# Kernel optimization log

Hardware: AMD Instinct MI355X
Metric: run time of the kernel (lower is better)

Reference implementation:

```python
import jax, jax.numpy as jnp
from jax import lax
import numpy as np

C_IN, D_INNER, D_STATE, OUT_CH = 20, 32, 8, 20
DT_RANK = max(1, D_INNER // 8)
B, H, W = 4, 384, 384
EPS = 1e-5


def layernorm(x, g, b):
    m = jnp.mean(x, axis=-1, keepdims=True)
    v = jnp.mean((x - m) ** 2, axis=-1, keepdims=True)
    return (x - m) * lax.rsqrt(v + EPS) * g + b


def ss1d(x, xw, dw, db, A_log, Dp):
    # x: (Bb, L, Dd). Mamba selective scan: h_t = exp(dt*A)*h_{t-1} + dt*B_t*u_t; y_t = C_t.h_t + D*u_t
    Bb, L, Dd = x.shape
    N = A_log.shape[1]
    xdbl = x @ xw.T                                   # (Bb, L, dtr+2N)
    dt_lo, Bm, Cm = jnp.split(xdbl, [DT_RANK, DT_RANK + N], axis=-1)
    dt = jax.nn.softplus(dt_lo @ dw.T + db)           # (Bb, L, Dd)
    A = -jnp.exp(A_log)                               # (Dd, N)

    def step(h, inp):
        dt_t, B_t, C_t, u_t = inp                     # (Bb,Dd),(Bb,N),(Bb,N),(Bb,Dd)
        dA = jnp.exp(dt_t[:, :, None] * A)            # (Bb, Dd, N)
        h = dA * h + (dt_t * u_t)[:, :, None] * B_t[:, None, :]
        y = jnp.einsum('bdn,bn->bd', h, C_t)
        return h, y

    xs = (jnp.moveaxis(dt, 1, 0), jnp.moveaxis(Bm, 1, 0),
          jnp.moveaxis(Cm, 1, 0), jnp.moveaxis(x, 1, 0))
    h0 = jnp.zeros((Bb, Dd, N), dtype=x.dtype)
    _, ys = lax.scan(step, h0, xs)
    return jnp.moveaxis(ys, 0, 1) + x * Dp


def setup_inputs() -> dict:
    key = jax.random.key(0)
    ks = jax.random.split(key, 16)
    s = lambda k, shp, sc=0.05: jax.random.normal(k, shp, dtype=jnp.float32) * sc
    A_log1 = jnp.log(jnp.broadcast_to(jnp.arange(1, D_STATE + 1, dtype=jnp.float32), (D_INNER, D_STATE)))
    return {
        'x': jax.random.normal(ks[0], (B, C_IN, H, W), dtype=jnp.float32),
        'norm_g': jnp.ones((C_IN,), jnp.float32),
        'norm_b': jnp.zeros((C_IN,), jnp.float32),
        'inproj_w': s(ks[1], (D_INNER, C_IN), 0.15),
        'dw_w': s(ks[2], (3, 3, 1, D_INNER), 0.2),
        'dw_b': jnp.zeros((D_INNER,), jnp.float32),
        'ssm_xw': s(ks[3], (4, DT_RANK + 2 * D_STATE, D_INNER), 0.1),
        'ssm_dw': s(ks[4], (4, D_INNER, DT_RANK), 0.5),
        'ssm_db': s(ks[5], (4, D_INNER), 0.5) - 3.0,
        'ssm_Alog': jnp.broadcast_to(A_log1, (4, D_INNER, D_STATE)).copy(),
        'ssm_D': jnp.ones((4, D_INNER), jnp.float32),
        'merge_g': jnp.ones((4 * D_INNER,), jnp.float32),
        'merge_b': jnp.zeros((4 * D_INNER,), jnp.float32),
        'merge_w': s(ks[6], (D_INNER, 4 * D_INNER), 0.1),
        'out_w': s(ks[7], (OUT_CH, D_INNER), 0.15),
        'out_b': jnp.zeros((OUT_CH,), jnp.float32),
    }


def reference(x, norm_g, norm_b, inproj_w, dw_w, dw_b, ssm_xw, ssm_dw, ssm_db,
              ssm_Alog, ssm_D, merge_g, merge_b, merge_w, out_w, out_b):
    Bx, C, Hx, Wx = x.shape
    h = jnp.transpose(x, (0, 2, 3, 1))                      # (B,H,W,C)
    h = layernorm(h, norm_g, norm_b)
    h = jax.nn.silu(h @ inproj_w.T)                          # (B,H,W,Dd)
    h = lax.conv_general_dilated(h, dw_w, (1, 1), 'SAME',
                                 dimension_numbers=('NHWC', 'HWIO', 'NHWC'),
                                 feature_group_count=D_INNER) + dw_b
    h = jax.nn.silu(h)                                       # (B,H,W,Dd)

    p = lambda i: (ssm_xw[i], ssm_dw[i], ssm_db[i], ssm_Alog[i], ssm_D[i])

    x_h = h.reshape(Bx * Hx, Wx, D_INNER)
    y_h_fwd = ss1d(x_h, *p(0)).reshape(Bx, Hx, Wx, D_INNER)
    y_h_bwd = ss1d(x_h[:, ::-1], *p(1))[:, ::-1].reshape(Bx, Hx, Wx, D_INNER)

    x_v = jnp.transpose(h, (0, 2, 1, 3)).reshape(Bx * Wx, Hx, D_INNER)
    y_v_fwd = jnp.transpose(ss1d(x_v, *p(2)).reshape(Bx, Wx, Hx, D_INNER), (0, 2, 1, 3))
    y_v_bwd = jnp.transpose(ss1d(x_v[:, ::-1], *p(3))[:, ::-1].reshape(Bx, Wx, Hx, D_INNER), (0, 2, 1, 3))

    y = jnp.concatenate([y_h_fwd, y_h_bwd, y_v_fwd, y_v_bwd], axis=-1)  # (B,H,W,4*Dd)
    y = layernorm(y, merge_g, merge_b)
    y = y @ merge_w.T                                        # (B,H,W,Dd)
    y = y @ out_w.T + out_b                                  # (B,H,W,out_ch)
    return jnp.transpose(y, (0, 3, 1, 2))                    # (B,out_ch,H,W)
```

## Files before the change

### kernel.cpp

```cpp
#include <hip/hip_runtime.h>

typedef unsigned short u16;
typedef unsigned int   u32;
typedef unsigned long long u64;
typedef float f2 __attribute__((ext_vector_type(2)));

#define CIN  20
#define DIN  32
#define BB   4
#define HH   384
#define WW   384
#define HW   147456
#define BHW  589824
#define EPSF 1e-5f
#define GUARD 65536

__device__ __forceinline__ float bflo(u32 u) {
    union { u32 v; float f; } x; x.v = u << 16; return x.f;
}
__device__ __forceinline__ float bfhi(u32 u) {
    union { u32 v; float f; } x; x.v = u & 0xffff0000u; return x.f;
}
__device__ __forceinline__ float bf2f(u16 h) {
    union { u32 v; float f; } x; x.v = ((u32)h) << 16; return x.f;
}
__device__ __forceinline__ u16 f2bf(float f) {
    union { float f; u32 u; } v; v.f = f;
    u32 u = v.u;
    return (u16)((u + 0x7FFFu + ((u >> 16) & 1u)) >> 16);
}
__device__ __forceinline__ float silu_f(float a) {
    return a / (1.f + __expf(-a));
}
__device__ __forceinline__ float softplus_f(float z) {
    return (z > 15.f) ? z : __logf(1.f + __expf(z));
}

__global__ void k_prep(const float* __restrict__ ow, const float* __restrict__ mw,
                       const float* __restrict__ mg, const float* __restrict__ mb,
                       const float* __restrict__ ob,
                       float* __restrict__ Wt, float* __restrict__ rsum,
                       float* __restrict__ c0)
{
    __shared__ float mdot[DIN];
    int t = threadIdx.x;
    if (t < DIN) {
        float s = 0.f;
        for (int k = 0; k < 128; ++k) s += mw[t*128 + k] * mb[k];
        mdot[t] = s;
    }
    {
        int k = t;
        for (int o = 0; o < CIN; ++o) {
            float s = 0.f;
            for (int d = 0; d < DIN; ++d) s += ow[o*DIN + d] * mw[d*128 + k];
            Wt[k*CIN + o] = s * mg[k];
        }
    }
    __syncthreads();
    if (t < CIN) {
        float rs = 0.f;
        for (int k = 0; k < 128; ++k) rs += Wt[k*CIN + t];
        rsum[t] = rs;
        float c = ob[t];
        for (int d = 0; d < DIN; ++d) c += ow[t*DIN + d] * mdot[d];
        c0[t] = c;
    }
}

__global__ __launch_bounds__(256) void k_lnproj(
    const float* __restrict__ x, const float* __restrict__ ng,
    const float* __restrict__ nb, const float* __restrict__ ipw,
    u16* __restrict__ h1)
{
    __shared__ float w_s[DIN*CIN];
    __shared__ float g_s[CIN], b_s[CIN];
    for (int i = threadIdx.x; i < DIN*CIN; i += 256) w_s[i] = ipw[i];
    if (threadIdx.x < CIN) { g_s[threadIdx.x] = ng[threadIdx.x]; b_s[threadIdx.x] = nb[threadIdx.x]; }
    __syncthreads();

    int p = blockIdx.x*256 + threadIdx.x;
    int b = p / HW, rem = p % HW;
    float v[CIN];
    float m = 0.f;
    #pragma unroll
    for (int c = 0; c < CIN; ++c) { v[c] = x[(b*CIN + c)*HW + rem]; m += v[c]; }
    m *= (1.f/CIN);
    float var = 0.f;
    #pragma unroll
    for (int c = 0; c < CIN; ++c) { float d = v[c]-m; var += d*d; }
    var *= (1.f/CIN);
    float rstd = rsqrtf(var + EPSF);
    #pragma unroll
    for (int c = 0; c < CIN; ++c) v[c] = (v[c]-m)*rstd*g_s[c] + b_s[c];

    float o[DIN];
    #pragma unroll
    for (int j = 0; j < DIN; ++j) {
        float acc = 0.f;
        #pragma unroll
        for (int c = 0; c < CIN; ++c) acc += w_s[j*CIN + c]*v[c];
        o[j] = silu_f(acc);
    }
    u32 pk[16];
    #pragma unroll
    for (int j2 = 0; j2 < 16; ++j2)
        pk[j2] = (u32)f2bf(o[2*j2]) | ((u32)f2bf(o[2*j2+1]) << 16);
    uint4* dst = (uint4*)(h1 + (size_t)p*DIN);
    dst[0] = make_uint4(pk[0],pk[1],pk[2],pk[3]);
    dst[1] = make_uint4(pk[4],pk[5],pk[6],pk[7]);
    dst[2] = make_uint4(pk[8],pk[9],pk[10],pk[11]);
    dst[3] = make_uint4(pk[12],pk[13],pk[14],pk[15]);
}

__global__ __launch_bounds__(256) void k_conv(
    const u16* __restrict__ h1, const float* __restrict__ cw,
    const float* __restrict__ cb, u16* __restrict__ h2)
{
    __shared__ float w_s[9*DIN];
    __shared__ float b_s[DIN];
    for (int i = threadIdx.x; i < 9*DIN; i += 256) w_s[i] = cw[i];
    if (threadIdx.x < DIN) b_s[threadIdx.x] = cb[threadIdx.x];
    __syncthreads();

    int tid = blockIdx.x*256 + threadIdx.x;
    int p = tid >> 2, g = tid & 3;
    int b = p / HW, rem = p % HW;
    int yy0 = rem / WW, xx0 = rem % WW;

    float acc[8];
    #pragma unroll
    for (int i = 0; i < 8; ++i) acc[i] = b_s[g*8 + i];

    #pragma unroll
    for (int dy = -1; dy <= 1; ++dy) {
        int yy = yy0 + dy;
        #pragma unroll
        for (int dx = -1; dx <= 1; ++dx) {
            int xc = xx0 + dx;
            if (yy >= 0 && yy < HH && xc >= 0 && xc < WW) {
                uint4 q = *(const uint4*)(h1 + ((size_t)(b*HW + yy*WW + xc)*DIN + g*8));
                int k = (dy+1)*3 + (dx+1);
                const float* wp = &w_s[k*DIN + g*8];
                acc[0] += wp[0]*bflo(q.x);  acc[1] += wp[1]*bfhi(q.x);
                acc[2] += wp[2]*bflo(q.y);  acc[3] += wp[3]*bfhi(q.y);
                acc[4] += wp[4]*bflo(q.z);  acc[5] += wp[5]*bfhi(q.z);
                acc[6] += wp[6]*bflo(q.w);  acc[7] += wp[7]*bfhi(q.w);
            }
        }
    }
    u32 pk[4];
    #pragma unroll
    for (int i2 = 0; i2 < 4; ++i2) {
        float a = silu_f(acc[2*i2]);
        float c = silu_f(acc[2*i2+1]);
        pk[i2] = (u32)f2bf(a) | ((u32)f2bf(c) << 16);
    }
    *(uint4*)(h2 + ((size_t)p*DIN + g*8)) = make_uint4(pk[0],pk[1],pk[2],pk[3]);
}

__global__ __launch_bounds__(256) void k_proj(
    const u16* __restrict__ h2, const float* __restrict__ xw,
    u16* __restrict__ dlA, u16* __restrict__ bcA)
{
    __shared__ float xw_s[4*CIN*DIN];
    for (int i = threadIdx.x; i < 4*CIN*DIN; i += 256) xw_s[i] = xw[i];
    __syncthreads();

    int p = blockIdx.x*256 + threadIdx.x;
    float u[DIN];
    const uint4* src = (const uint4*)(h2 + (size_t)p*DIN);
    #pragma unroll
    for (int q4 = 0; q4 < 4; ++q4) {
        uint4 v = src[q4];
        u[q4*8+0]=bflo(v.x); u[q4*8+1]=bfhi(v.x);
        u[q4*8+2]=bflo(v.y); u[q4*8+3]=bfhi(v.y);
        u[q4*8+4]=bflo(v.z); u[q4*8+5]=bfhi(v.z);
        u[q4*8+6]=bflo(v.w); u[q4*8+7]=bfhi(v.w);
    }
    #pragma unroll 1
    for (int dir = 0; dir < 4; ++dir) {
        float xd[CIN];
        #pragma unroll
        for (int j = 0; j < CIN; ++j) xd[j] = 0.f;
        #pragma unroll
        for (int d4 = 0; d4 < 8; ++d4) {
            float u0 = u[d4*4], u1 = u[d4*4+1], u2 = u[d4*4+2], u3 = u[d4*4+3];
            #pragma unroll
            for (int j = 0; j < CIN; ++j) {
                float4 w4 = *(const float4*)&xw_s[(dir*CIN + j)*DIN + d4*4];
                xd[j] += w4.x*u0 + w4.y*u1 + w4.z*u2 + w4.w*u3;
            }
        }
        u32 pk[10];
        #pragma unroll
        for (int i = 0; i < 10; ++i)
            pk[i] = (u32)f2bf(xd[2*i]) | ((u32)f2bf(xd[2*i+1]) << 16);
        *(uint2*)(dlA + (size_t)(dir*BHW + p)*4) = make_uint2(pk[0], pk[1]);
        uint4* bcd = (uint4*)(bcA + (size_t)(dir*BHW + p)*16);
        bcd[0] = make_uint4(pk[2], pk[3], pk[4], pk[5]);
        bcd[1] = make_uint4(pk[6], pk[7], pk[8], pk[9]);
    }
}

__global__ __launch_bounds__(256) void k_scan(
    const char* __restrict__ h2b,
    const char* __restrict__ dlb_,
    const char* __restrict__ bcb_,
    const float* __restrict__ Alog, const float* __restrict__ Dp,
    const float* __restrict__ dwm,  const float* __restrict__ dbv,
    char* __restrict__ y4b)
{
    int tid  = blockIdx.x*256 + threadIdx.x;
    int wv   = tid >> 6, lane = tid & 63;
    int half = lane >> 5, d = lane & 31;
    int dir  = wv / 768;
    int s    = (wv % 768)*2 + half;
    int b    = s / 384, r = s % 384;

    int p0, stp;
    if (dir == 0)      { p0 = b*HW + r*WW;           stp = 1;  }
    else if (dir == 1) { p0 = b*HW + r*WW + (WW-1);  stp = -1; }
    else if (dir == 2) { p0 = b*HW + r;              stp = WW; }
    else               { p0 = b*HW + (HH-1)*WW + r;  stp = -WW;}

    float Av[8];
    bool okl = true;
    #pragma unroll
    for (int j = 0; j < 8; ++j) {
        float e = __expf(Alog[(dir*DIN + d)*8 + j]);
        Av[j] = -e;
        okl = okl && (__builtin_fabsf(e - (float)(j+1)) < 2e-3f);
    }
    bool fast = (__ballot(okl) == ~0ull);

    float Dd  = Dp[dir*DIN + d];
    float dw0 = dwm[(dir*DIN + d)*4 + 0], dw1 = dwm[(dir*DIN + d)*4 + 1];
    float dw2 = dwm[(dir*DIN + d)*4 + 2], dw3 = dwm[(dir*DIN + d)*4 + 3];
    float dbc = dbv[dir*DIN + d];

    u32 uo = GUARD + (u32)((p0*DIN + d)*2);            int su = stp*DIN*2;
    u32 yo = (u32)((dir*BHW + p0)*64 + d*2);           int sy = stp*64;
    u32 c1 = GUARD + (u32)((dir*BHW + p0)*8);          int s1 = stp*8;
    u32 c2 = GUARD + (u32)((dir*BHW + p0)*32);         int s2 = stp*32;

    u16 ub[2]; uint2 dlr[2]; uint4 B4[2], C4[2];
    u32 fu = uo, f1 = c1, f2o = c2;

    auto fetch = [&](int sl) {
        ub[sl]  = *(const u16*)(h2b + fu);
        dlr[sl] = *(const uint2*)(dlb_ + f1);
        B4[sl]  = *(const uint4*)(bcb_ + f2o);
        C4[sl]  = *(const uint4*)(bcb_ + f2o + 16);
        fu += (u32)su; f1 += (u32)s1; f2o += (u32)s2;
    };

    fetch(0); fetch(1);

    f2 h0 = {0.f,0.f}, h1 = {0.f,0.f}, h2v = {0.f,0.f}, h3 = {0.f,0.f};

    if (fast) {
        #pragma unroll 2
        for (int t = 0; t < 384; ++t) {
            int sl = t & 1;
            float uu = bf2f(ub[sl]);
            uint2 dl = dlr[sl];
            uint4 Bv = B4[sl], Cv = C4[sl];
            fetch(sl);

            float z = dbc + dw0*bflo(dl.x) + dw1*bfhi(dl.x)
                          + dw2*bflo(dl.y) + dw3*bfhi(dl.y);
            z = fminf(z, 80.f);
            float rr = __builtin_amdgcn_rcpf(1.f + __expf(z));
            float dt = -__logf(rr);
            float r2 = rr*rr;
            f2 rr2 = {r2, r2};
            f2 a01 = {rr, r2};
            f2 a23 = a01*rr2;
            f2 a45 = a23*rr2;
            f2 a67 = a45*rr2;

            float dtu = dt*uu;
            f2 du2 = {dtu, dtu};
            f2 Bp0 = { bflo(Bv.x), bfhi(Bv.x) }, Bp1 = { bflo(Bv.y), bfhi(Bv.y) };
            f2 Bp2 = { bflo(Bv.z), bfhi(Bv.z) }, Bp3 = { bflo(Bv.w), bfhi(Bv.w) };
            f2 Cp0 = { bflo(Cv.x), bfhi(Cv.x) }, Cp1 = { bflo(Cv.y), bfhi(Cv.y) };
            f2 Cp2 = { bflo(Cv.z), bfhi(Cv.z) }, Cp3 = { bflo(Cv.w), bfhi(Cv.w) };

            h0  = __builtin_elementwise_fma(a01, h0,  du2*Bp0);
            h1  = __builtin_elementwise_fma(a23, h1,  du2*Bp1);
            h2v = __builtin_elementwise_fma(a45, h2v, du2*Bp2);
            h3  = __builtin_elementwise_fma(a67, h3,  du2*Bp3);

            f2 yv = Cp0*h0;
            yv = __builtin_elementwise_fma(Cp1, h1,  yv);
            yv = __builtin_elementwise_fma(Cp2, h2v, yv);
            yv = __builtin_elementwise_fma(Cp3, h3,  yv);

            float y = yv.x + yv.y + Dd*uu;
            *(u16*)(y4b + yo) = f2bf(y);
            yo += (u32)sy;
        }
    } else {
        f2 A2[4];
        #pragma unroll
        for (int j = 0; j < 4; ++j) { A2[j].x = Av[2*j]; A2[j].y = Av[2*j+1]; }
        #pragma unroll 2
        for (int t = 0; t < 384; ++t) {
            int sl = t & 1;
            float uu = bf2f(ub[sl]);
            uint2 dl = dlr[sl];
            uint4 Bv = B4[sl], Cv = C4[sl];
            fetch(sl);

            float z = dbc + dw0*bflo(dl.x) + dw1*bfhi(dl.x)
                          + dw2*bflo(dl.y) + dw3*bfhi(dl.y);
            float dt = softplus_f(z);
            f2 dt2 = {dt, dt};
            f2 e0 = dt2*A2[0], e1 = dt2*A2[1], e2 = dt2*A2[2], e3 = dt2*A2[3];
            f2 a01 = { __expf(e0.x), __expf(e0.y) };
            f2 a23 = { __expf(e1.x), __expf(e1.y) };
            f2 a45 = { __expf(e2.x), __expf(e2.y) };
            f2 a67 = { __expf(e3.x), __expf(e3.y) };

            float dtu = dt*uu;
            f2 du2 = {dtu, dtu};
            f2 Bp0 = { bflo(Bv.x), bfhi(Bv.x) }, Bp1 = { bflo(Bv.y), bfhi(Bv.y) };
            f2 Bp2 = { bflo(Bv.z), bfhi(Bv.z) }, Bp3 = { bflo(Bv.w), bfhi(Bv.w) };
            f2 Cp0 = { bflo(Cv.x), bfhi(Cv.x) }, Cp1 = { bflo(Cv.y), bfhi(Cv.y) };
            f2 Cp2 = { bflo(Cv.z), bfhi(Cv.z) }, Cp3 = { bflo(Cv.w), bfhi(Cv.w) };

            h0  = __builtin_elementwise_fma(a01, h0,  du2*Bp0);
            h1  = __builtin_elementwise_fma(a23, h1,  du2*Bp1);
            h2v = __builtin_elementwise_fma(a45, h2v, du2*Bp2);
            h3  = __builtin_elementwise_fma(a67, h3,  du2*Bp3);

            f2 yv = Cp0*h0;
            yv = __builtin_elementwise_fma(Cp1, h1,  yv);
            yv = __builtin_elementwise_fma(Cp2, h2v, yv);
            yv = __builtin_elementwise_fma(Cp3, h3,  yv);

            float y = yv.x + yv.y + Dd*uu;
            *(u16*)(y4b + yo) = f2bf(y);
            yo += (u32)sy;
        }
    }
}

__global__ __launch_bounds__(256) void k_merge(
    const u16* __restrict__ y4, const float* __restrict__ Wt,
    const float* __restrict__ rsum, const float* __restrict__ c0,
    float* __restrict__ out)
{
    __shared__ float Wt_s[128*CIN];
    __shared__ float rs_s[CIN], c0_s[CIN];
    for (int i = threadIdx.x; i < 128*CIN; i += 256) Wt_s[i] = Wt[i];
    if (threadIdx.x < CIN) { rs_s[threadIdx.x] = rsum[threadIdx.x]; c0_s[threadIdx.x] = c0[threadIdx.x]; }
    __syncthreads();

    int p = blockIdx.x*256 + threadIdx.x;
    int b = p / HW, rem = p % HW;

    float s1 = 0.f, s2 = 0.f;
    float acc[CIN];
    #pragma unroll
    for (int o = 0; o < CIN; ++o) acc[o] = 0.f;

    #pragma unroll 1
    for (int dirk = 0; dirk < 4; ++dirk) {
        const uint4* src = (const uint4*)(y4 + ((size_t)dirk*BHW + p)*32);
        #pragma unroll
        for (int q4 = 0; q4 < 4; ++q4) {
            uint4 v = src[q4];
            u32 w[4] = {v.x, v.y, v.z, v.w};
            #pragma unroll
            for (int i = 0; i < 4; ++i) {
                int k = dirk*32 + q4*8 + i*2;
                float a = bflo(w[i]); float c = bfhi(w[i]);
                s1 += a + c; s2 += a*a + c*c;
                const float4* w0 = (const float4*)&Wt_s[k*CIN];
                const float4* w1 = (const float4*)&Wt_s[(k+1)*CIN];
                #pragma unroll
                for (int o4 = 0; o4 < 5; ++o4) {
                    float4 x0 = w0[o4], x1 = w1[o4];
                    acc[o4*4+0] += x0.x*a + x1.x*c;
                    acc[o4*4+1] += x0.y*a + x1.y*c;
                    acc[o4*4+2] += x0.z*a + x1.z*c;
                    acc[o4*4+3] += x0.w*a + x1.w*c;
                }
            }
        }
    }
    float m = s1*(1.f/128.f);
    float var = s2*(1.f/128.f) - m*m;
    float rstd = rsqrtf(var + EPSF);
    #pragma unroll
    for (int o = 0; o < CIN; ++o) {
        float res = rstd*(acc[o] - m*rs_s[o]) + c0_s[o];
        out[(b*CIN + o)*HW + rem] = res;
    }
}

extern "C" void kernel_launch(void* const* d_in, const int* in_sizes, int n_in,
                              void* d_out, int out_size, void* d_ws, size_t ws_size,
                              hipStream_t stream)
{
    const float* x    = (const float*)d_in[0];
    const float* ng   = (const float*)d_in[1];
    const float* nb   = (const float*)d_in[2];
    const float* ipw  = (const float*)d_in[3];
    const float* cw   = (const float*)d_in[4];
    const float* cb   = (const float*)d_in[5];
    const float* xw   = (const float*)d_in[6];
    const float* dwm  = (const float*)d_in[7];
    const float* dbv  = (const float*)d_in[8];
    const float* Alog = (const float*)d_in[9];
    const float* Dpv  = (const float*)d_in[10];
    const float* mg   = (const float*)d_in[11];
    const float* mb   = (const float*)d_in[12];
    const float* mw   = (const float*)d_in[13];
    const float* ow   = (const float*)d_in[14];
    const float* ob   = (const float*)d_in[15];
    float* out = (float*)d_out;

    const size_t y4_bytes = (size_t)4*BHW*DIN*2;
    const size_t dl_bytes = (size_t)4*BHW*8;
    const size_t bc_bytes = (size_t)4*BHW*32;
    const size_t wt_bytes = (size_t)(128*CIN + 64)*4;

    char* ws = (char*)d_ws;
    u16* y4 = (u16*)ws;
    u16* h1 = y4;

    size_t dl_pos = y4_bytes + GUARD;
    size_t bc_pos = dl_pos + dl_bytes + GUARD;
    size_t wt_pos = bc_pos + bc_bytes + GUARD;
    size_t need   = wt_pos + wt_bytes + GUARD;

    if (ws_size < need) {
        hipMemsetAsync(d_out, 0x7F, (size_t)out_size*4, stream);
        return;
    }

    char* h2base = (char*)d_out;
    u16*  h2 = (u16*)(h2base + GUARD);

    u16* dlA = (u16*)(ws + dl_pos);
    u16* bcA = (u16*)(ws + bc_pos);
    float* Wt   = (float*)(ws + wt_pos);
    float* rsum = Wt + 128*CIN;
    float* c0   = rsum + 32;

    k_prep  <<<1, 128, 0, stream>>>(ow, mw, mg, mb, ob, Wt, rsum, c0);
    k_lnproj<<<BHW/256, 256, 0, stream>>>(x, ng, nb, ipw, h1);
    k_conv  <<<BHW*4/256, 256, 0, stream>>>(h1, cw, cb, h2);
    k_proj  <<<BHW/256, 256, 0, stream>>>(h2, xw, dlA, bcA);
    k_scan  <<<768, 256, 0, stream>>>(
        h2base, (const char*)(ws + dl_pos - GUARD), (const char*)(ws + bc_pos - GUARD),
        Alog, Dpv, dwm, dbv, (char*)y4);
    k_merge <<<BHW/256, 256, 0, stream>>>(y4, Wt, rsum, c0, out);
}
```

Before: 530.3 us.

## Use MFMA bf16 for merge projection and interleave scan dt/B/C records

```diff
diff --git a/kernel.cpp b/kernel.cpp
--- a/kernel.cpp
+++ b/kernel.cpp
@@ -4,6 +4,8 @@
 typedef unsigned int   u32;
 typedef unsigned long long u64;
 typedef float f2 __attribute__((ext_vector_type(2)));
+typedef __attribute__((ext_vector_type(8))) short s8v;
+typedef __attribute__((ext_vector_type(4))) float f4v;
 
 #define CIN  20
 #define DIN  32
@@ -29,6 +31,9 @@
     u32 u = v.u;
     return (u16)((u + 0x7FFFu + ((u >> 16) & 1u)) >> 16);
 }
+__device__ __forceinline__ u32 pk2(float a, float b) {
+    return (u32)f2bf(a) | ((u32)f2bf(b) << 16);
+}
 __device__ __forceinline__ float silu_f(float a) {
     return a / (1.f + __expf(-a));
 }
@@ -40,7 +45,7 @@
                        const float* __restrict__ mg, const float* __restrict__ mb,
                        const float* __restrict__ ob,
                        float* __restrict__ Wt, float* __restrict__ rsum,
-                       float* __restrict__ c0)
+                       float* __restrict__ c0, u16* __restrict__ Bfr)
 {
     __shared__ float mdot[DIN];
     int t = threadIdx.x;
@@ -66,6 +71,16 @@
         for (int d = 0; d < DIN; ++d) c += ow[t*DIN + d] * mdot[d];
         c0[t] = c;
     }
+    for (int i = t; i < 4096; i += 128) {
+        int j    = i & 7;
+        int lane = (i >> 3) & 63;
+        int dir  = (i >> 9) & 3;
+        int tile = i >> 11;
+        int o = tile*16 + (lane & 15);
+        int k = dir*32 + ((lane >> 4) & 3)*8 + j;
+        float v = (o < CIN) ? Wt[k*CIN + o] : 0.f;
+        Bfr[i] = f2bf(v);
+    }
 }
 
 __global__ __launch_bounds__(256) void k_lnproj(
@@ -105,7 +120,7 @@
     u32 pk[16];
     #pragma unroll
     for (int j2 = 0; j2 < 16; ++j2)
-        pk[j2] = (u32)f2bf(o[2*j2]) | ((u32)f2bf(o[2*j2+1]) << 16);
+        pk[j2] = pk2(o[2*j2], o[2*j2+1]);
     uint4* dst = (uint4*)(h1 + (size_t)p*DIN);
     dst[0] = make_uint4(pk[0],pk[1],pk[2],pk[3]);
     dst[1] = make_uint4(pk[4],pk[5],pk[6],pk[7]);
@@ -159,6 +174,7 @@
     *(uint4*)(h2 + ((size_t)p*DIN + g*8)) = make_uint4(pk[0],pk[1],pk[2],pk[3]);
 }
 
+template<bool COMB>
 __global__ __launch_bounds__(256) void k_proj(
     const u16* __restrict__ h2, const float* __restrict__ xw,
     u16* __restrict__ dlA, u16* __restrict__ bcA)
@@ -195,18 +211,26 @@
         u32 pk[10];
         #pragma unroll
         for (int i = 0; i < 10; ++i)
-            pk[i] = (u32)f2bf(xd[2*i]) | ((u32)f2bf(xd[2*i+1]) << 16);
-        *(uint2*)(dlA + (size_t)(dir*BHW + p)*4) = make_uint2(pk[0], pk[1]);
-        uint4* bcd = (uint4*)(bcA + (size_t)(dir*BHW + p)*16);
-        bcd[0] = make_uint4(pk[2], pk[3], pk[4], pk[5]);
-        bcd[1] = make_uint4(pk[6], pk[7], pk[8], pk[9]);
-    }
-}
-
+            pk[i] = pk2(xd[2*i], xd[2*i+1]);
+        if (COMB) {
+            u16* rp = dlA + (size_t)(dir*BHW + p)*24;
+            *(uint4*)(rp)      = make_uint4(pk[2],pk[3],pk[4],pk[5]);
+            *(uint4*)(rp + 8)  = make_uint4(pk[6],pk[7],pk[8],pk[9]);
+            *(uint2*)(rp + 16) = make_uint2(pk[0], pk[1]);
+        } else {
+            *(uint2*)(dlA + (size_t)(dir*BHW + p)*4) = make_uint2(pk[0], pk[1]);
+            uint4* bcd = (uint4*)(bcA + (size_t)(dir*BHW + p)*16);
+            bcd[0] = make_uint4(pk[2], pk[3], pk[4], pk[5]);
+            bcd[1] = make_uint4(pk[6], pk[7], pk[8], pk[9]);
+        }
+    }
+}
+
+template<bool COMB>
 __global__ __launch_bounds__(256) void k_scan(
     const char* __restrict__ h2b,
-    const char* __restrict__ dlb_,
-    const char* __restrict__ bcb_,
+    const char* __restrict__ s1b,
+    const char* __restrict__ s2b,
     const float* __restrict__ Alog, const float* __restrict__ Dp,
     const float* __restrict__ dwm,  const float* __restrict__ dbv,
     char* __restrict__ y4b)
@@ -241,163 +265,170 @@
 
     u32 uo = GUARD + (u32)((p0*DIN + d)*2);            int su = stp*DIN*2;
     u32 yo = (u32)((dir*BHW + p0)*64 + d*2);           int sy = stp*64;
-    u32 c1 = GUARD + (u32)((dir*BHW + p0)*8);          int s1 = stp*8;
-    u32 c2 = GUARD + (u32)((dir*BHW + p0)*32);         int s2 = stp*32;
+    u32 c1, c2 = 0; int st1, st2 = 0;
+    if (COMB) { c1 = GUARD + (u32)((dir*BHW + p0)*48); st1 = stp*48; }
+    else {
+        c1 = GUARD + (u32)((dir*BHW + p0)*8);          st1 = stp*8;
+        c2 = GUARD + (u32)((dir*BHW + p0)*32);         st2 = stp*32;
+    }
 
     u16 ub[2]; uint2 dlr[2]; uint4 B4[2], C4[2];
     u32 fu = uo, f1 = c1, f2o = c2;
 
     auto fetch = [&](int sl) {
         ub[sl]  = *(const u16*)(h2b + fu);
-        dlr[sl] = *(const uint2*)(dlb_ + f1);
-        B4[sl]  = *(const uint4*)(bcb_ + f2o);
-        C4[sl]  = *(const uint4*)(bcb_ + f2o + 16);
-        fu += (u32)su; f1 += (u32)s1; f2o += (u32)s2;
+        if (COMB) {
+            B4[sl]  = *(const uint4*)(s1b + f1);
+            C4[sl]  = *(const uint4*)(s1b + f1 + 16);
+            dlr[sl] = *(const uint2*)(s1b + f1 + 32);
+        } else {
+            dlr[sl] = *(const uint2*)(s1b + f1);
+            B4[sl]  = *(const uint4*)(s2b + f2o);
+            C4[sl]  = *(const uint4*)(s2b + f2o + 16);
+            f2o += (u32)st2;
+        }
+        fu += (u32)su; f1 += (u32)st1;
     };
 
     fetch(0); fetch(1);
 
     f2 h0 = {0.f,0.f}, h1 = {0.f,0.f}, h2v = {0.f,0.f}, h3 = {0.f,0.f};
 
-    if (fast) {
-        #pragma unroll 2
-        for (int t = 0; t < 384; ++t) {
-            int sl = t & 1;
-            float uu = bf2f(ub[sl]);
-            uint2 dl = dlr[sl];
-            uint4 Bv = B4[sl], Cv = C4[sl];
-            fetch(sl);
-
-            float z = dbc + dw0*bflo(dl.x) + dw1*bfhi(dl.x)
-                          + dw2*bflo(dl.y) + dw3*bfhi(dl.y);
+    #pragma unroll 2
+    for (int t = 0; t < 384; ++t) {
+        int sl = t & 1;
+        float uu = bf2f(ub[sl]);
+        uint2 dl = dlr[sl];
+        uint4 Bv = B4[sl], Cv = C4[sl];
+        fetch(sl);
+
+        float z = dbc + dw0*bflo(dl.x) + dw1*bfhi(dl.x)
+                      + dw2*bflo(dl.y) + dw3*bfhi(dl.y);
+        f2 a01, a23, a45, a67;
+        float dt;
+        if (fast) {
             z = fminf(z, 80.f);
             float rr = __builtin_amdgcn_rcpf(1.f + __expf(z));
-            float dt = -__logf(rr);
+            dt = -__logf(rr);
             float r2 = rr*rr;
             f2 rr2 = {r2, r2};
-            f2 a01 = {rr, r2};
-            f2 a23 = a01*rr2;
-            f2 a45 = a23*rr2;
-            f2 a67 = a45*rr2;
-
-            float dtu = dt*uu;
-            f2 du2 = {dtu, dtu};
-            f2 Bp0 = { bflo(Bv.x), bfhi(Bv.x) }, Bp1 = { bflo(Bv.y), bfhi(Bv.y) };
-            f2 Bp2 = { bflo(Bv.z), bfhi(Bv.z) }, Bp3 = { bflo(Bv.w), bfhi(Bv.w) };
-            f2 Cp0 = { bflo(Cv.x), bfhi(Cv.x) }, Cp1 = { bflo(Cv.y), bfhi(Cv.y) };
-            f2 Cp2 = { bflo(Cv.z), bfhi(Cv.z) }, Cp3 = { bflo(Cv.w), bfhi(Cv.w) };
-
-            h0  = __builtin_elementwise_fma(a01, h0,  du2*Bp0);
-            h1  = __builtin_elementwise_fma(a23, h1,  du2*Bp1);
-            h2v = __builtin_elementwise_fma(a45, h2v, du2*Bp2);
-            h3  = __builtin_elementwise_fma(a67, h3,  du2*Bp3);
-
-            f2 yv = Cp0*h0;
-            yv = __builtin_elementwise_fma(Cp1, h1,  yv);
-            yv = __builtin_elementwise_fma(Cp2, h2v, yv);
-            yv = __builtin_elementwise_fma(Cp3, h3,  yv);
-
-            float y = yv.x + yv.y + Dd*uu;
-            *(u16*)(y4b + yo) = f2bf(y);
-            yo += (u32)sy;
-        }
-    } else {
-        f2 A2[4];
-        #pragma unroll
-        for (int j = 0; j < 4; ++j) { A2[j].x = Av[2*j]; A2[j].y = Av[2*j+1]; }
-        #pragma unroll 2
-        for (int t = 0; t < 384; ++t) {
-            int sl = t & 1;
-            float uu = bf2f(ub[sl]);
-            uint2 dl = dlr[sl];
-            uint4 Bv = B4[sl], Cv = C4[sl];
-            fetch(sl);
-
-            float z = dbc + dw0*bflo(dl.x) + dw1*bfhi(dl.x)
-                          + dw2*bflo(dl.y) + dw3*bfhi(dl.y);
-            float dt = softplus_f(z);
+            a01 = f2{rr, r2};
+            a23 = a01*rr2;
+            a45 = a23*rr2;
+            a67 = a45*rr2;
+        } else {
+            dt = softplus_f(z);
             f2 dt2 = {dt, dt};
-            f2 e0 = dt2*A2[0], e1 = dt2*A2[1], e2 = dt2*A2[2], e3 = dt2*A2[3];
-            f2 a01 = { __expf(e0.x), __expf(e0.y) };
-            f2 a23 = { __expf(e1.x), __expf(e1.y) };
-            f2 a45 = { __expf(e2.x), __expf(e2.y) };
-            f2 a67 = { __expf(e3.x), __expf(e3.y) };
-
-            float dtu = dt*uu;
-            f2 du2 = {dtu, dtu};
-            f2 Bp0 = { bflo(Bv.x), bfhi(Bv.x) }, Bp1 = { bflo(Bv.y), bfhi(Bv.y) };
-            f2 Bp2 = { bflo(Bv.z), bfhi(Bv.z) }, Bp3 = { bflo(Bv.w), bfhi(Bv.w) };
-            f2 Cp0 = { bflo(Cv.x), bfhi(Cv.x) }, Cp1 = { bflo(Cv.y), bfhi(Cv.y) };
-            f2 Cp2 = { bflo(Cv.z), bfhi(Cv.z) }, Cp3 = { bflo(Cv.w), bfhi(Cv.w) };
-
-            h0  = __builtin_elementwise_fma(a01, h0,  du2*Bp0);
-            h1  = __builtin_elementwise_fma(a23, h1,  du2*Bp1);
-            h2v = __builtin_elementwise_fma(a45, h2v, du2*Bp2);
-            h3  = __builtin_elementwise_fma(a67, h3,  du2*Bp3);
-
-            f2 yv = Cp0*h0;
-            yv = __builtin_elementwise_fma(Cp1, h1,  yv);
-            yv = __builtin_elementwise_fma(Cp2, h2v, yv);
-            yv = __builtin_elementwise_fma(Cp3, h3,  yv);
-
-            float y = yv.x + yv.y + Dd*uu;
-            *(u16*)(y4b + yo) = f2bf(y);
-            yo += (u32)sy;
-        }
-    }
-}
-
-__global__ __launch_bounds__(256) void k_merge(
-    const u16* __restrict__ y4, const float* __restrict__ Wt,
+            f2 e0 = dt2*f2{Av[0],Av[1]}, e1 = dt2*f2{Av[2],Av[3]};
+            f2 e2 = dt2*f2{Av[4],Av[5]}, e3 = dt2*f2{Av[6],Av[7]};
+            a01 = f2{ __expf(e0.x), __expf(e0.y) };
+            a23 = f2{ __expf(e1.x), __expf(e1.y) };
+            a45 = f2{ __expf(e2.x), __expf(e2.y) };
+            a67 = f2{ __expf(e3.x), __expf(e3.y) };
+        }
+
+        f2 Bp0 = f2{ bflo(Bv.x), bfhi(Bv.x) }, Bp1 = f2{ bflo(Bv.y), bfhi(Bv.y) };
+        f2 Bp2 = f2{ bflo(Bv.z), bfhi(Bv.z) }, Bp3 = f2{ bflo(Bv.w), bfhi(Bv.w) };
+        f2 Cp0 = f2{ bflo(Cv.x), bfhi(Cv.x) }, Cp1 = f2{ bflo(Cv.y), bfhi(Cv.y) };
+        f2 Cp2 = f2{ bflo(Cv.z), bfhi(Cv.z) }, Cp3 = f2{ bflo(Cv.w), bfhi(Cv.w) };
+
+        float dtu = dt*uu;
+        f2 du2 = {dtu, dtu};
+
+        h0  = __builtin_elementwise_fma(a01, h0,  du2*Bp0);
+        h1  = __builtin_elementwise_fma(a23, h1,  du2*Bp1);
+        h2v = __builtin_elementwise_fma(a45, h2v, du2*Bp2);
+        h3  = __builtin_elementwise_fma(a67, h3,  du2*Bp3);
+
+        f2 yv = Cp0*h0;
+        yv = __builtin_elementwise_fma(Cp1, h1,  yv);
+        yv = __builtin_elementwise_fma(Cp2, h2v, yv);
+        yv = __builtin_elementwise_fma(Cp3, h3,  yv);
+
+        float y = yv.x + yv.y + Dd*uu;
+        *(u16*)(y4b + yo) = f2bf(y);
+        yo += (u32)sy;
+    }
+}
+
+__global__ __launch_bounds__(256) void k_merge_m(
+    const u16* __restrict__ y4, const u16* __restrict__ bfr,
     const float* __restrict__ rsum, const float* __restrict__ c0,
     float* __restrict__ out)
 {
-    __shared__ float Wt_s[128*CIN];
-    __shared__ float rs_s[CIN], c0_s[CIN];
-    for (int i = threadIdx.x; i < 128*CIN; i += 256) Wt_s[i] = Wt[i];
-    if (threadIdx.x < CIN) { rs_s[threadIdx.x] = rsum[threadIdx.x]; c0_s[threadIdx.x] = c0[threadIdx.x]; }
-    __syncthreads();
-
-    int p = blockIdx.x*256 + threadIdx.x;
-    int b = p / HW, rem = p % HW;
-
-    float s1 = 0.f, s2 = 0.f;
-    float acc[CIN];
-    #pragma unroll
-    for (int o = 0; o < CIN; ++o) acc[o] = 0.f;
+    int w = threadIdx.x >> 6, lane = threadIdx.x & 63;
+    int quad = lane >> 4, mcol = lane & 15;
+
+    s8v bf[2][4];
+    #pragma unroll
+    for (int tile = 0; tile < 2; ++tile)
+        #pragma unroll
+        for (int dir = 0; dir < 4; ++dir)
+            bf[tile][dir] = *(const s8v*)(bfr + ((size_t)((tile*4+dir)*64 + lane))*8);
+
+    int o0 = mcol, o1 = 16 + mcol;
+    float rs0 = rsum[o0], cc0 = c0[o0];
+    float rs1 = (o1 < CIN) ? rsum[o1] : 0.f;
+    float cc1 = (o1 < CIN) ? c0[o1] : 0.f;
+
+    int pxblock = blockIdx.x*256 + w*64;
+    int b = pxblock / HW, rem0 = pxblock % HW;
 
     #pragma unroll 1
-    for (int dirk = 0; dirk < 4; ++dirk) {
-        const uint4* src = (const uint4*)(y4 + ((size_t)dirk*BHW + p)*32);
-        #pragma unroll
-        for (int q4 = 0; q4 < 4; ++q4) {
-            uint4 v = src[q4];
-            u32 w[4] = {v.x, v.y, v.z, v.w};
+    for (int tt = 0; tt < 4; ++tt) {
+        int px = pxblock + tt*16 + mcol;
+        uint4 aw[4]; s8v af[4];
+        f2 s1v = {0.f,0.f}, s2v = {0.f,0.f};
+        #pragma unroll
+        for (int dir = 0; dir < 4; ++dir) {
+            aw[dir] = *(const uint4*)(y4 + ((size_t)dir*BHW + px)*32 + quad*8);
+            af[dir] = __builtin_bit_cast(s8v, aw[dir]);
+            u32 ww[4] = {aw[dir].x, aw[dir].y, aw[dir].z, aw[dir].w};
             #pragma unroll
             for (int i = 0; i < 4; ++i) {
-                int k = dirk*32 + q4*8 + i*2;
-                float a = bflo(w[i]); float c = bfhi(w[i]);
-                s1 += a + c; s2 += a*a + c*c;
-                const float4* w0 = (const float4*)&Wt_s[k*CIN];
-                const float4* w1 = (const float4*)&Wt_s[(k+1)*CIN];
-                #pragma unroll
-                for (int o4 = 0; o4 < 5; ++o4) {
-                    float4 x0 = w0[o4], x1 = w1[o4];
-                    acc[o4*4+0] += x0.x*a + x1.x*c;
-                    acc[o4*4+1] += x0.y*a + x1.y*c;
-                    acc[o4*4+2] += x0.z*a + x1.z*c;
-                    acc[o4*4+3] += x0.w*a + x1.w*c;
-                }
+                f2 v = { bflo(ww[i]), bfhi(ww[i]) };
+                s1v = s1v + v;
+                s2v = __builtin_elementwise_fma(v, v, s2v);
             }
         }
-    }
-    float m = s1*(1.f/128.f);
-    float var = s2*(1.f/128.f) - m*m;
-    float rstd = rsqrtf(var + EPSF);
-    #pragma unroll
-    for (int o = 0; o < CIN; ++o) {
-        float res = rstd*(acc[o] - m*rs_s[o]) + c0_s[o];
-        out[(b*CIN + o)*HW + rem] = res;
+        float s1 = s1v.x + s1v.y, s2 = s2v.x + s2v.y;
+        s1 += __shfl_xor(s1, 16, 64); s2 += __shfl_xor(s2, 16, 64);
+        s1 += __shfl_xor(s1, 32, 64); s2 += __shfl_xor(s2, 32, 64);
+        float mu   = s1*(1.f/128.f);
+        float var  = s2*(1.f/128.f) - mu*mu;
+        float rstd = rsqrtf(var + EPSF);
+
+        f4v acc0 = {0.f,0.f,0.f,0.f}, acc1 = {0.f,0.f,0.f,0.f};
+        #pragma unroll
+        for (int dir = 0; dir < 4; ++dir) {
+            acc0 = __builtin_amdgcn_mfma_f32_16x16x32_bf16(af[dir], bf[0][dir], acc0, 0, 0, 0);
+            acc1 = __builtin_amdgcn_mfma_f32_16x16x32_bf16(af[dir], bf[1][dir], acc1, 0, 0, 0);
+        }
+
+        float mur[4], rsr[4];
+        #pragma unroll
+        for (int rg = 0; rg < 4; ++rg) {
+            int row = quad*4 + rg;
+            mur[rg] = __shfl(mu,   row, 64);
+            rsr[rg] = __shfl(rstd, row, 64);
+        }
+        int rembase = rem0 + tt*16 + quad*4;
+        {
+            float4 o4;
+            o4.x = rsr[0]*(acc0.x - mur[0]*rs0) + cc0;
+            o4.y = rsr[1]*(acc0.y - mur[1]*rs0) + cc0;
+            o4.z = rsr[2]*(acc0.z - mur[2]*rs0) + cc0;
+            o4.w = rsr[3]*(acc0.w - mur[3]*rs0) + cc0;
+            *(float4*)(out + (size_t)(b*CIN + o0)*HW + rembase) = o4;
+        }
+        if (o1 < CIN) {
+            float4 o4;
+            o4.x = rsr[0]*(acc1.x - mur[0]*rs1) + cc1;
+            o4.y = rsr[1]*(acc1.y - mur[1]*rs1) + cc1;
+            o4.z = rsr[2]*(acc1.z - mur[2]*rs1) + cc1;
+            o4.w = rsr[3]*(acc1.w - mur[3]*rs1) + cc1;
+            *(float4*)(out + (size_t)(b*CIN + o1)*HW + rembase) = o4;
+        }
     }
 }
 
@@ -423,40 +454,56 @@
     const float* ob   = (const float*)d_in[15];
     float* out = (float*)d_out;
 
-    const size_t y4_bytes = (size_t)4*BHW*DIN*2;
-    const size_t dl_bytes = (size_t)4*BHW*8;
-    const size_t bc_bytes = (size_t)4*BHW*32;
-    const size_t wt_bytes = (size_t)(128*CIN + 64)*4;
+    const size_t y4_bytes  = (size_t)4*BHW*DIN*2;
+    const size_t dl_bytes  = (size_t)4*BHW*8;
+    const size_t bc_bytes  = (size_t)4*BHW*32;
+    const size_t rec_bytes = (size_t)4*BHW*48;
+    const size_t wt_bytes  = 10240 + 256 + 8192;
 
     char* ws = (char*)d_ws;
     u16* y4 = (u16*)ws;
     u16* h1 = y4;
 
-    size_t dl_pos = y4_bytes + GUARD;
-    size_t bc_pos = dl_pos + dl_bytes + GUARD;
-    size_t wt_pos = bc_pos + bc_bytes + GUARD;
-    size_t need   = wt_pos + wt_bytes + GUARD;
-
-    if (ws_size < need) {
+    size_t s1_pos = y4_bytes + GUARD;
+    size_t bc_pos       = s1_pos + dl_bytes + GUARD;
+    size_t wt_pos_split = bc_pos + bc_bytes + GUARD;
+    size_t need_split   = wt_pos_split + wt_bytes + GUARD;
+    size_t wt_pos_comb  = s1_pos + rec_bytes + GUARD;
+    size_t need_comb    = wt_pos_comb + wt_bytes + GUARD;
+
+    if (ws_size < need_split) {
         hipMemsetAsync(d_out, 0x7F, (size_t)out_size*4, stream);
         return;
     }
+    bool comb = (ws_size >= need_comb);
 
     char* h2base = (char*)d_out;
     u16*  h2 = (u16*)(h2base + GUARD);
 
-    u16* dlA = (u16*)(ws + dl_pos);
-    u16* bcA = (u16*)(ws + bc_pos);
+    size_t wt_pos = comb ? wt_pos_comb : wt_pos_split;
     float* Wt   = (float*)(ws + wt_pos);
     float* rsum = Wt + 128*CIN;
     float* c0   = rsum + 32;
-
-    k_prep  <<<1, 128, 0, stream>>>(ow, mw, mg, mb, ob, Wt, rsum, c0);
+    u16*   Bfr  = (u16*)(ws + wt_pos + 10240 + 256);
+
+    k_prep  <<<1, 128, 0, stream>>>(ow, mw, mg, mb, ob, Wt, rsum, c0, Bfr);
     k_lnproj<<<BHW/256, 256, 0, stream>>>(x, ng, nb, ipw, h1);
     k_conv  <<<BHW*4/256, 256, 0, stream>>>(h1, cw, cb, h2);
-    k_proj  <<<BHW/256, 256, 0, stream>>>(h2, xw, dlA, bcA);
-    k_scan  <<<768, 256, 0, stream>>>(
-        h2base, (const char*)(ws + dl_pos - GUARD), (const char*)(ws + bc_pos - GUARD),
-        Alog, Dpv, dwm, dbv, (char*)y4);
-    k_merge <<<BHW/256, 256, 0, stream>>>(y4, Wt, rsum, c0, out);
-}
+
+    if (comb) {
+        u16* rec = (u16*)(ws + s1_pos);
+        k_proj<true><<<BHW/256, 256, 0, stream>>>(h2, xw, rec, nullptr);
+        k_scan<true><<<768, 256, 0, stream>>>(
+            h2base, (const char*)(ws + s1_pos - GUARD), nullptr,
+            Alog, Dpv, dwm, dbv, (char*)y4);
+    } else {
+        u16* dlA = (u16*)(ws + s1_pos);
+        u16* bcA = (u16*)(ws + bc_pos);
+        k_proj<false><<<BHW/256, 256, 0, stream>>>(h2, xw, dlA, bcA);
+        k_scan<false><<<768, 256, 0, stream>>>(
+            h2base, (const char*)(ws + s1_pos - GUARD), (const char*)(ws + bc_pos - GUARD),
+            Alog, Dpv, dwm, dbv, (char*)y4);
+    }
+
+    k_merge_m<<<BHW/256, 256, 0, stream>>>(y4, Bfr, rsum, c0, out);
+}
```

New measurement: 559.8 us. 1.06x slower.
